# Kernel tuning notes

Hardware: AMD Instinct MI355X
Metric: run time of the kernel (lower is better)

The kernel has to match this reference:

```python
import jax, jax.numpy as jnp
import numpy as np

B, N, T, D = 256, 64, 60, 128
H = 128  # gate hidden dims


def setup_inputs() -> dict:
    key = jax.random.key(0)
    ks = jax.random.split(key, 5)
    x = jax.random.normal(ks[0], (B, N, T, D), dtype=jnp.float32)
    s = 1.0 / np.sqrt(D)
    sg_w1 = jax.random.normal(ks[1], (D, H), dtype=jnp.float32) * s
    sg_b1 = jnp.zeros((H,), dtype=jnp.float32)
    sg_w2 = jax.random.normal(ks[2], (H, 1), dtype=jnp.float32) * (1.0 / np.sqrt(H))
    sg_b2 = jnp.zeros((1,), dtype=jnp.float32)
    tg_w1 = jax.random.normal(ks[3], (D, H), dtype=jnp.float32) * s
    tg_b1 = jnp.zeros((H,), dtype=jnp.float32)
    tg_w2 = jax.random.normal(ks[4], (H, 1), dtype=jnp.float32) * (1.0 / np.sqrt(H))
    tg_b2 = jnp.zeros((1,), dtype=jnp.float32)
    return {"x": x, "sg_w1": sg_w1, "sg_b1": sg_b1, "sg_w2": sg_w2, "sg_b2": sg_b2,
            "tg_w1": tg_w1, "tg_b1": tg_b1, "tg_w2": tg_w2, "tg_b2": tg_b2}


def reference(x, sg_w1, sg_b1, sg_w2, sg_b2, tg_w1, tg_b1, tg_w2, tg_b2):
    # Spatial attentional aggregation, vectorized over all timesteps at once.
    # Segment softmax over batch_index == softmax over the node axis (regular segments).
    gate = jnp.tanh(x @ sg_w1 + sg_b1) @ sg_w2 + sg_b2          # [B, N, T, 1]
    alpha = jax.nn.softmax(gate, axis=1)                        # softmax over nodes
    pooled = jnp.sum(alpha * x, axis=1)                         # [B, T, D]
    # Temporal attention pooling over the sequence axis.
    score = jnp.tanh(pooled @ tg_w1 + tg_b1) @ tg_w2 + tg_b2    # [B, T, 1]
    tw = jax.nn.softmax(score, axis=1)                          # [B, T, 1]
    final = jnp.sum(tw * pooled, axis=1)                        # [B, D]
    return final, tw
```

## Files before the change

kernel.cpp:

```cpp
#include <hip/hip_runtime.h>

#define B_ 256
#define N_ 64
#define T_ 60
#define D_ 128
#define H_ 128

typedef __attribute__((ext_vector_type(8))) short short8;
typedef __attribute__((ext_vector_type(4))) float f32x4;

__device__ __forceinline__ unsigned short f2bf(float f) {
  unsigned int u = __builtin_bit_cast(unsigned int, f);
  u = u + 0x7FFFu + ((u >> 16) & 1u);
  return (unsigned short)(u >> 16);
}

__device__ __forceinline__ float tanh_fast(float x) {
  float e = __builtin_amdgcn_exp2f(x * 2.885390081777927f);
  return 1.0f - 2.0f * __builtin_amdgcn_rcpf(e + 1.0f);
}

__global__ __launch_bounds__(256) void prep_weights(
    const float* __restrict__ sg_w1, const float* __restrict__ tg_w1,
    unsigned short* __restrict__ wfrag) {
  int tid = blockIdx.x * 256 + threadIdx.x;
  if (tid >= 2 * 4 * 8 * 64) return;
  int l  = tid & 63;
  int nt = (tid >> 6) & 7;
  int kt = (tid >> 9) & 3;
  int m  = tid >> 11;
  const float* W = m ? tg_w1 : sg_w1;
  int n  = nt * 16 + (l & 15);
  int k0 = kt * 32 + 8 * (l >> 4);
  unsigned short* dst = wfrag + (size_t)tid * 8;
#pragma unroll
  for (int i = 0; i < 8; ++i) dst[i] = f2bf(W[(k0 + i) * H_ + n]);
}

__global__ __launch_bounds__(256, 4) void spatial_kernel(
    const float* __restrict__ x,
    const short8* __restrict__ wfrag,
    const float* __restrict__ b1,
    const float* __restrict__ w2,
    float* __restrict__ pooled) {
  __shared__ __align__(16) char xs16[64 * 272];
  __shared__ float gpart[2][64];

  const int tid = threadIdx.x;
  const int bid = blockIdx.x;
  const int b = bid / T_;
  const int t = bid - b * T_;

  const float* xb = x + (size_t)b * (N_ * T_ * D_) + (size_t)t * D_;

  const int cg  = tid >> 3;
  const int sub = tid & 7;

  float4 px[8];
#pragma unroll
  for (int r = 0; r < 8; ++r) {
    const int n = sub + 8 * r;
    px[r] = *(const float4*)(xb + (size_t)n * (T_ * D_) + 4 * cg);
  }
#pragma unroll
  for (int r = 0; r < 8; ++r) {
    const int n = sub + 8 * r;
    unsigned lo = ((unsigned)f2bf(px[r].y) << 16) | f2bf(px[r].x);
    unsigned hi = ((unsigned)f2bf(px[r].w) << 16) | f2bf(px[r].z);
    *(uint2*)(xs16 + n * 272 + cg * 8) = make_uint2(lo, hi);
  }
  __syncthreads();

  const int l  = tid & 63;
  const int w  = tid >> 6;
  const int lg = l >> 4;
  const int lr = l & 15;
  const int wr = w >> 1;
  const int wc = w & 1;

  float b1v[4], w2v[4];
#pragma unroll
  for (int ntl = 0; ntl < 4; ++ntl) {
    b1v[ntl] = b1[wc * 64 + ntl * 16 + lr];
    w2v[ntl] = w2[wc * 64 + ntl * 16 + lr];
  }

  f32x4 acc[2][4];
#pragma unroll
  for (int mt = 0; mt < 2; ++mt)
#pragma unroll
    for (int ntl = 0; ntl < 4; ++ntl) acc[mt][ntl] = (f32x4)(0.0f);

#pragma unroll
  for (int kt = 0; kt < 4; ++kt) {
#pragma unroll
    for (int mt = 0; mt < 2; ++mt) {
      const int row = 32 * wr + 16 * mt + lr;
      short8 af = *(const short8*)(xs16 + row * 272 + kt * 64 + lg * 16);
#pragma unroll
      for (int ntl = 0; ntl < 4; ++ntl) {
        short8 bf = wfrag[(kt * 8 + wc * 4 + ntl) * 64 + l];
        acc[mt][ntl] = __builtin_amdgcn_mfma_f32_16x16x32_bf16(af, bf, acc[mt][ntl], 0, 0, 0);
      }
    }
  }

#pragma unroll
  for (int mt = 0; mt < 2; ++mt) {
#pragma unroll
    for (int j = 0; j < 4; ++j) {
      float s = 0.f;
#pragma unroll
      for (int ntl = 0; ntl < 4; ++ntl) {
        float h = acc[mt][ntl][j] + b1v[ntl];
        s += tanh_fast(h) * w2v[ntl];
      }
      s += __shfl_xor(s, 1);
      s += __shfl_xor(s, 2);
      s += __shfl_xor(s, 4);
      s += __shfl_xor(s, 8);
      if (lr == 0) gpart[wc][32 * wr + 16 * mt + 4 * lg + j] = s;
    }
  }
  __syncthreads();

  float g = gpart[0][l] + gpart[1][l];
  float p = __builtin_amdgcn_exp2f(g * 1.4426950408889634f);
  float sm = p;
  sm += __shfl_xor(sm, 32);
  sm += __shfl_xor(sm, 16);
  sm += __shfl_xor(sm, 8);
  sm += __shfl_xor(sm, 4);
  sm += __shfl_xor(sm, 2);
  sm += __shfl_xor(sm, 1);
  const float alpha = p * __builtin_amdgcn_rcpf(sm);

  f32x4 q = (f32x4)(0.0f);
#pragma unroll
  for (int r = 0; r < 8; ++r) {
    const int n = sub + 8 * r;
    const float av = __shfl(alpha, n);
    q[0] += av * px[r].x;
    q[1] += av * px[r].y;
    q[2] += av * px[r].z;
    q[3] += av * px[r].w;
  }
#pragma unroll
  for (int m = 1; m <= 4; m <<= 1) {
    q[0] += __shfl_xor(q[0], m);
    q[1] += __shfl_xor(q[1], m);
    q[2] += __shfl_xor(q[2], m);
    q[3] += __shfl_xor(q[3], m);
  }
  if (sub == 0)
    *(f32x4*)(pooled + ((size_t)b * T_ + t) * D_ + 4 * cg) = q;
}

__global__ __launch_bounds__(256) void temporal_kernel(
    const float* __restrict__ pooled,
    const short8* __restrict__ wfrag,
    const float* __restrict__ b1,
    const float* __restrict__ w2,
    float* __restrict__ out) {
  __shared__ float xs[64][132];
  __shared__ float score_lds[64];
  __shared__ float tw_lds[64];
  __shared__ float pp[2][128];

  const int tid = threadIdx.x;
  const int b = blockIdx.x;

  const float* pb = pooled + (size_t)b * T_ * D_;
#pragma unroll
  for (int it = 0; it < 8; ++it) {
    int q = it * 256 + tid;
    int n = q >> 5;
    int c4 = (q & 31) << 2;
    float4 v = {0.f, 0.f, 0.f, 0.f};
    if (n < T_) v = *(const float4*)(pb + n * D_ + c4);
    *(float4*)(&xs[n][c4]) = v;
  }
  __syncthreads();

  const int l = tid & 63;
  const int w = tid >> 6;
  const int lg = l >> 4;
  const int lr = l & 15;

  float b1v[8], w2v[8];
#pragma unroll
  for (int nt = 0; nt < 8; ++nt) {
    b1v[nt] = b1[nt * 16 + lr];
    w2v[nt] = w2[nt * 16 + lr];
  }

  f32x4 acc[8];
#pragma unroll
  for (int nt = 0; nt < 8; ++nt) acc[nt] = (f32x4)(0.0f);

  const int row = 16 * w + lr;
#pragma unroll
  for (int kt = 0; kt < 4; ++kt) {
    const int k0 = kt * 32 + 8 * lg;
    float4 a0 = *(const float4*)(&xs[row][k0]);
    float4 a1 = *(const float4*)(&xs[row][k0 + 4]);
    short8 af;
    af[0] = (short)f2bf(a0.x); af[1] = (short)f2bf(a0.y);
    af[2] = (short)f2bf(a0.z); af[3] = (short)f2bf(a0.w);
    af[4] = (short)f2bf(a1.x); af[5] = (short)f2bf(a1.y);
    af[6] = (short)f2bf(a1.z); af[7] = (short)f2bf(a1.w);
#pragma unroll
    for (int nt = 0; nt < 8; ++nt) {
      short8 bf = wfrag[(kt * 8 + nt) * 64 + l];
      acc[nt] = __builtin_amdgcn_mfma_f32_16x16x32_bf16(af, bf, acc[nt], 0, 0, 0);
    }
  }

#pragma unroll
  for (int j = 0; j < 4; ++j) {
    float s = 0.f;
#pragma unroll
    for (int nt = 0; nt < 8; ++nt) {
      float h = acc[nt][j] + b1v[nt];
      s += tanh_fast(h) * w2v[nt];
    }
    s += __shfl_xor(s, 1);
    s += __shfl_xor(s, 2);
    s += __shfl_xor(s, 4);
    s += __shfl_xor(s, 8);
    if (lr == 0) score_lds[16 * w + 4 * lg + j] = s;
  }
  __syncthreads();

  float p = (l < T_) ? __builtin_amdgcn_exp2f(score_lds[l] * 1.4426950408889634f) : 0.f;
  float sm = p;
  sm += __shfl_xor(sm, 32);
  sm += __shfl_xor(sm, 16);
  sm += __shfl_xor(sm, 8);
  sm += __shfl_xor(sm, 4);
  sm += __shfl_xor(sm, 2);
  sm += __shfl_xor(sm, 1);
  float tw = p / sm;
  if (w == 0) {
    tw_lds[l] = tw;
    if (l < T_) out[B_ * D_ + b * T_ + l] = tw;
  }
  __syncthreads();

  const int c = tid & 127;
  const int hh = tid >> 7;
  float s = 0.f;
#pragma unroll
  for (int i = 0; i < 30; ++i) {
    int tt = 30 * hh + i;
    s += tw_lds[tt] * xs[tt][c];
  }
  pp[hh][c] = s;
  __syncthreads();
  if (tid < 128) out[(size_t)b * D_ + tid] = pp[0][tid] + pp[1][tid];
}

extern "C" void kernel_launch(void* const* d_in, const int* in_sizes, int n_in,
                              void* d_out, int out_size, void* d_ws, size_t ws_size,
                              hipStream_t stream) {
  const float* x     = (const float*)d_in[0];
  const float* sg_w1 = (const float*)d_in[1];
  const float* sg_b1 = (const float*)d_in[2];
  const float* sg_w2 = (const float*)d_in[3];
  const float* tg_w1 = (const float*)d_in[5];
  const float* tg_b1 = (const float*)d_in[6];
  const float* tg_w2 = (const float*)d_in[7];
  float* out = (float*)d_out;

  unsigned short* wfrag = (unsigned short*)d_ws;
  float* pooled = (float*)((char*)d_ws + 65536);

  prep_weights<<<16, 256, 0, stream>>>(sg_w1, tg_w1, wfrag);
  spatial_kernel<<<B_ * T_, 256, 0, stream>>>(
      x, (const short8*)wfrag, sg_b1, sg_w2, pooled);
  temporal_kernel<<<B_, 256, 0, stream>>>(
      pooled, (const short8*)(wfrag + 16384), tg_b1, tg_w2, out);
}
```

Measured before the change: 154.1 us.

## Process two timesteps per spatial block with contiguous 1KB row loads

Each spatial block now handles two adjacent timesteps with 512 threads, so every wave loads a full contiguous 1KB span (two t rows × 128 floats) per node instead of 512B fragments. Grid size is halved and the per-timestep work is split across wave groups. The shuffle-based alpha broadcast and cross-lane reduction are replaced by LDS arrays and a cross-wave reduction through shared memory. This adds LDS usage and extra barriers, which may reduce occupancy.

```diff
diff --git a/kernel.cpp b/kernel.cpp
--- a/kernel.cpp
+++ b/kernel.cpp
@@ -37,45 +37,46 @@
   for (int i = 0; i < 8; ++i) dst[i] = f2bf(W[(k0 + i) * H_ + n]);
 }
 
-__global__ __launch_bounds__(256, 4) void spatial_kernel(
+__global__ __launch_bounds__(512, 4) void spatial_kernel(
     const float* __restrict__ x,
     const short8* __restrict__ wfrag,
     const float* __restrict__ b1,
     const float* __restrict__ w2,
     float* __restrict__ pooled) {
-  __shared__ __align__(16) char xs16[64 * 272];
-  __shared__ float gpart[2][64];
+  __shared__ __align__(16) char xt16[2 * 17408];
+  __shared__ float gpart[2][2][64];
+  __shared__ float alph[2][64];
+  __shared__ f32x4 pp[8][64];
 
   const int tid = threadIdx.x;
   const int bid = blockIdx.x;
-  const int b = bid / T_;
-  const int t = bid - b * T_;
-
-  const float* xb = x + (size_t)b * (N_ * T_ * D_) + (size_t)t * D_;
-
-  const int cg  = tid >> 3;
-  const int sub = tid & 7;
-
+  const int b  = bid / (T_ / 2);
+  const int tc = bid - b * (T_ / 2);
+  const int t0 = 2 * tc;
+
+  const int w = tid >> 6;
+  const int l = tid & 63;
+
+  const float* xb = x + (size_t)b * (N_ * T_ * D_) + (size_t)t0 * D_;
   float4 px[8];
 #pragma unroll
-  for (int r = 0; r < 8; ++r) {
-    const int n = sub + 8 * r;
-    px[r] = *(const float4*)(xb + (size_t)n * (T_ * D_) + 4 * cg);
-  }
-#pragma unroll
-  for (int r = 0; r < 8; ++r) {
-    const int n = sub + 8 * r;
-    unsigned lo = ((unsigned)f2bf(px[r].y) << 16) | f2bf(px[r].x);
-    unsigned hi = ((unsigned)f2bf(px[r].w) << 16) | f2bf(px[r].z);
-    *(uint2*)(xs16 + n * 272 + cg * 8) = make_uint2(lo, hi);
-  }
-  __syncthreads();
-
-  const int l  = tid & 63;
-  const int w  = tid >> 6;
+  for (int j = 0; j < 8; ++j)
+    px[j] = *(const float4*)(xb + (size_t)(8 * j + w) * (T_ * D_) + 4 * l);
+
+  const int lt  = l >> 5;
+  const int d4  = l & 31;
+#pragma unroll
+  for (int j = 0; j < 8; ++j) {
+    unsigned lo = ((unsigned)f2bf(px[j].y) << 16) | f2bf(px[j].x);
+    unsigned hi = ((unsigned)f2bf(px[j].w) << 16) | f2bf(px[j].z);
+    *(uint2*)(xt16 + lt * 17408 + (8 * j + w) * 272 + d4 * 8) = make_uint2(lo, hi);
+  }
+  __syncthreads();
+
   const int lg = l >> 4;
   const int lr = l & 15;
-  const int wr = w >> 1;
+  const int tw = w >> 2;
+  const int wr = (w >> 1) & 1;
   const int wc = w & 1;
 
   float b1v[4], w2v[4];
@@ -96,7 +97,7 @@
 #pragma unroll
     for (int mt = 0; mt < 2; ++mt) {
       const int row = 32 * wr + 16 * mt + lr;
-      short8 af = *(const short8*)(xs16 + row * 272 + kt * 64 + lg * 16);
+      short8 af = *(const short8*)(xt16 + tw * 17408 + row * 272 + kt * 64 + lg * 16);
 #pragma unroll
       for (int ntl = 0; ntl < 4; ++ntl) {
         short8 bf = wfrag[(kt * 8 + wc * 4 + ntl) * 64 + l];
@@ -119,41 +120,43 @@
       s += __shfl_xor(s, 2);
       s += __shfl_xor(s, 4);
       s += __shfl_xor(s, 8);
-      if (lr == 0) gpart[wc][32 * wr + 16 * mt + 4 * lg + j] = s;
-    }
-  }
-  __syncthreads();
-
-  float g = gpart[0][l] + gpart[1][l];
-  float p = __builtin_amdgcn_exp2f(g * 1.4426950408889634f);
-  float sm = p;
-  sm += __shfl_xor(sm, 32);
-  sm += __shfl_xor(sm, 16);
-  sm += __shfl_xor(sm, 8);
-  sm += __shfl_xor(sm, 4);
-  sm += __shfl_xor(sm, 2);
-  sm += __shfl_xor(sm, 1);
-  const float alpha = p * __builtin_amdgcn_rcpf(sm);
+      if (lr == 0) gpart[tw][wc][32 * wr + 16 * mt + 4 * lg + j] = s;
+    }
+  }
+  __syncthreads();
+
+  if ((w & 3) == 0) {
+    float g = gpart[tw][0][l] + gpart[tw][1][l];
+    float p = __builtin_amdgcn_exp2f(g * 1.4426950408889634f);
+    float sm = p;
+    sm += __shfl_xor(sm, 32);
+    sm += __shfl_xor(sm, 16);
+    sm += __shfl_xor(sm, 8);
+    sm += __shfl_xor(sm, 4);
+    sm += __shfl_xor(sm, 2);
+    sm += __shfl_xor(sm, 1);
+    alph[tw][l] = p * __builtin_amdgcn_rcpf(sm);
+  }
+  __syncthreads();
 
   f32x4 q = (f32x4)(0.0f);
 #pragma unroll
-  for (int r = 0; r < 8; ++r) {
-    const int n = sub + 8 * r;
-    const float av = __shfl(alpha, n);
-    q[0] += av * px[r].x;
-    q[1] += av * px[r].y;
-    q[2] += av * px[r].z;
-    q[3] += av * px[r].w;
-  }
-#pragma unroll
-  for (int m = 1; m <= 4; m <<= 1) {
-    q[0] += __shfl_xor(q[0], m);
-    q[1] += __shfl_xor(q[1], m);
-    q[2] += __shfl_xor(q[2], m);
-    q[3] += __shfl_xor(q[3], m);
-  }
-  if (sub == 0)
-    *(f32x4*)(pooled + ((size_t)b * T_ + t) * D_ + 4 * cg) = q;
+  for (int j = 0; j < 8; ++j) {
+    const float av = alph[lt][8 * j + w];
+    q[0] += av * px[j].x;
+    q[1] += av * px[j].y;
+    q[2] += av * px[j].z;
+    q[3] += av * px[j].w;
+  }
+  pp[w][l] = q;
+  __syncthreads();
+
+  if (w == 0) {
+    f32x4 s4 = pp[0][l];
+#pragma unroll
+    for (int w2i = 1; w2i < 8; ++w2i) s4 += pp[w2i][l];
+    *(f32x4*)(pooled + ((size_t)b * T_ + t0 + lt) * D_ + 4 * d4) = s4;
+  }
 }
 
 __global__ __launch_bounds__(256) void temporal_kernel(
@@ -276,7 +279,7 @@
   float* pooled = (float*)((char*)d_ws + 65536);
 
   prep_weights<<<16, 256, 0, stream>>>(sg_w1, tg_w1, wfrag);
-  spatial_kernel<<<B_ * T_, 256, 0, stream>>>(
+  spatial_kernel<<<B_ * (T_ / 2), 512, 0, stream>>>(
       x, (const short8*)wfrag, sg_b1, sg_w2, pooled);
   temporal_kernel<<<B_, 256, 0, stream>>>(
       pooled, (const short8*)(wfrag + 16384), tg_b1, tg_w2, out);
```

New measurement: 150.3 us. 2.5% less time.

## Restructure spatial kernel into per-batch node-slab loop with streaming softmax

Applied to the files above, without the earlier changes.

Each spatial block now handles one batch and half of the nodes (32 slabs), iterating over node slabs where each slab covers all 60 timesteps. The next slab's x loads are double-buffered against the current MFMA and gating work. The softmax becomes an unnormalized exp-weighted accumulation with the denominator stored separately. The temporal kernel merges the two halves and normalizes. Gate weights are staged once in LDS per block instead of being re-read from global memory per timestep block. The grid shrinks from 15360 blocks to 512 with more sequential work each, which risks low occupancy/parallelism (2 blocks per CU). Dropping max-subtraction in the softmax risks overflow.

```diff
diff --git a/kernel.cpp b/kernel.cpp
--- a/kernel.cpp
+++ b/kernel.cpp
@@ -18,6 +18,12 @@
 __device__ __forceinline__ float tanh_fast(float x) {
   float e = __builtin_amdgcn_exp2f(x * 2.885390081777927f);
   return 1.0f - 2.0f * __builtin_amdgcn_rcpf(e + 1.0f);
+}
+
+__device__ __forceinline__ void lds_barrier() {
+  asm volatile("s_waitcnt lgkmcnt(0)" ::: "memory");
+  __builtin_amdgcn_s_barrier();
+  asm volatile("" ::: "memory");
 }
 
 __global__ __launch_bounds__(256) void prep_weights(
@@ -37,39 +43,33 @@
   for (int i = 0; i < 8; ++i) dst[i] = f2bf(W[(k0 + i) * H_ + n]);
 }
 
-__global__ __launch_bounds__(256, 4) void spatial_kernel(
+__global__ __launch_bounds__(256, 2) void spatial_kernel(
     const float* __restrict__ x,
-    const short8* __restrict__ wfrag,
+    const unsigned short* __restrict__ wfrag_g,
     const float* __restrict__ b1,
     const float* __restrict__ w2,
-    float* __restrict__ pooled) {
-  __shared__ __align__(16) char xs16[64 * 272];
+    float* __restrict__ acc_p,
+    float* __restrict__ den_p) {
+  __shared__ __align__(16) char tile[64 * 272];
+  __shared__ __align__(16) char wlds[32768];
   __shared__ float gpart[2][64];
 
   const int tid = threadIdx.x;
   const int bid = blockIdx.x;
-  const int b = bid / T_;
-  const int t = bid - b * T_;
-
-  const float* xb = x + (size_t)b * (N_ * T_ * D_) + (size_t)t * D_;
-
-  const int cg  = tid >> 3;
-  const int sub = tid & 7;
-
-  float4 px[8];
+  const int b  = bid >> 1;
+  const int nh = bid & 1;
+
+  const int sub = tid >> 5;
+  const int cg  = tid & 31;
+
+  const float* xb = x + (size_t)b * (N_ * T_ * D_) + (size_t)(nh * 32) * (T_ * D_);
+
+  int roff[8];
 #pragma unroll
   for (int r = 0; r < 8; ++r) {
-    const int n = sub + 8 * r;
-    px[r] = *(const float4*)(xb + (size_t)n * (T_ * D_) + 4 * cg);
-  }
-#pragma unroll
-  for (int r = 0; r < 8; ++r) {
-    const int n = sub + 8 * r;
-    unsigned lo = ((unsigned)f2bf(px[r].y) << 16) | f2bf(px[r].x);
-    unsigned hi = ((unsigned)f2bf(px[r].w) << 16) | f2bf(px[r].z);
-    *(uint2*)(xs16 + n * 272 + cg * 8) = make_uint2(lo, hi);
-  }
-  __syncthreads();
+    int t = 8 * r + sub;
+    roff[r] = (t > 59 ? 59 : t) * D_ + 4 * cg;
+  }
 
   const int l  = tid & 63;
   const int w  = tid >> 6;
@@ -85,79 +85,119 @@
     w2v[ntl] = w2[wc * 64 + ntl * 16 + lr];
   }
 
-  f32x4 acc[2][4];
-#pragma unroll
-  for (int mt = 0; mt < 2; ++mt)
-#pragma unroll
-    for (int ntl = 0; ntl < 4; ++ntl) acc[mt][ntl] = (f32x4)(0.0f);
-
-#pragma unroll
-  for (int kt = 0; kt < 4; ++kt) {
-#pragma unroll
-    for (int mt = 0; mt < 2; ++mt) {
-      const int row = 32 * wr + 16 * mt + lr;
-      short8 af = *(const short8*)(xs16 + row * 272 + kt * 64 + lg * 16);
-#pragma unroll
-      for (int ntl = 0; ntl < 4; ++ntl) {
-        short8 bf = wfrag[(kt * 8 + wc * 4 + ntl) * 64 + l];
-        acc[mt][ntl] = __builtin_amdgcn_mfma_f32_16x16x32_bf16(af, bf, acc[mt][ntl], 0, 0, 0);
-      }
-    }
-  }
-
-#pragma unroll
-  for (int mt = 0; mt < 2; ++mt) {
-#pragma unroll
-    for (int j = 0; j < 4; ++j) {
-      float s = 0.f;
-#pragma unroll
-      for (int ntl = 0; ntl < 4; ++ntl) {
-        float h = acc[mt][ntl][j] + b1v[ntl];
-        s += tanh_fast(h) * w2v[ntl];
-      }
-      s += __shfl_xor(s, 1);
-      s += __shfl_xor(s, 2);
-      s += __shfl_xor(s, 4);
-      s += __shfl_xor(s, 8);
-      if (lr == 0) gpart[wc][32 * wr + 16 * mt + 4 * lg + j] = s;
-    }
-  }
-  __syncthreads();
-
-  float g = gpart[0][l] + gpart[1][l];
-  float p = __builtin_amdgcn_exp2f(g * 1.4426950408889634f);
-  float sm = p;
-  sm += __shfl_xor(sm, 32);
-  sm += __shfl_xor(sm, 16);
-  sm += __shfl_xor(sm, 8);
-  sm += __shfl_xor(sm, 4);
-  sm += __shfl_xor(sm, 2);
-  sm += __shfl_xor(sm, 1);
-  const float alpha = p * __builtin_amdgcn_rcpf(sm);
-
-  f32x4 q = (f32x4)(0.0f);
+  float4 wtmp[8];
+#pragma unroll
+  for (int i = 0; i < 8; ++i)
+    wtmp[i] = *(const float4*)(wfrag_g + (size_t)(tid + 256 * i) * 8);
+
+  float4 pxA[8], pxB[8];
+#pragma unroll
+  for (int r = 0; r < 8; ++r) pxA[r] = *(const float4*)(xb + roff[r]);
+
+#pragma unroll
+  for (int i = 0; i < 8; ++i)
+    *(float4*)(wlds + (size_t)(tid + 256 * i) * 16) = wtmp[i];
+  lds_barrier();
+
+  f32x4 accr[8];
+  float denr[8];
+#pragma unroll
+  for (int r = 0; r < 8; ++r) { accr[r] = (f32x4)(0.0f); denr[r] = 0.0f; }
+
+#define SLAB_BODY(CUR, NXT, S)                                                  \
+  {                                                                             \
+                   \
+    if ((S) < 31) {                                                             \
+      const float* nsb = xb + (size_t)((S) + 1) * (T_ * D_);                    \
+      _Pragma("unroll")                                                         \
+      for (int r = 0; r < 8; ++r) NXT[r] = *(const float4*)(nsb + roff[r]);     \
+    }                                                                           \
+                                               \
+    _Pragma("unroll")                                                           \
+    for (int r = 0; r < 8; ++r) {                                               \
+      const int t = 8 * r + sub;                                                \
+      unsigned lo = ((unsigned)f2bf(CUR[r].y) << 16) | f2bf(CUR[r].x);          \
+      unsigned hi = ((unsigned)f2bf(CUR[r].w) << 16) | f2bf(CUR[r].z);          \
+      *(uint2*)(tile + t * 272 + cg * 8) = make_uint2(lo, hi);                  \
+    }                                                                           \
+    lds_barrier();                                                              \
+                           \
+    {                                                                           \
+      f32x4 macc[2][4];                                                         \
+      _Pragma("unroll")                                                         \
+      for (int mt = 0; mt < 2; ++mt)                                            \
+        _Pragma("unroll")                                                       \
+        for (int ntl = 0; ntl < 4; ++ntl) macc[mt][ntl] = (f32x4)(0.0f);        \
+      _Pragma("unroll")                                                         \
+      for (int kt = 0; kt < 4; ++kt) {                                          \
+        _Pragma("unroll")                                                       \
+        for (int mt = 0; mt < 2; ++mt) {                                        \
+          const int row = 32 * wr + 16 * mt + lr;                               \
+          short8 af = *(const short8*)(tile + row * 272 + kt * 64 + lg * 16);   \
+          _Pragma("unroll")                                                     \
+          for (int ntl = 0; ntl < 4; ++ntl) {                                   \
+            short8 bf = *(const short8*)(                                       \
+                wlds + ((kt * 8 + wc * 4 + ntl) * 64 + l) * 16);                \
+            macc[mt][ntl] = __builtin_amdgcn_mfma_f32_16x16x32_bf16(            \
+                af, bf, macc[mt][ntl], 0, 0, 0);                                \
+          }                                                                     \
+        }                                                                       \
+      }                                                                         \
+      _Pragma("unroll")                                                         \
+      for (int mt = 0; mt < 2; ++mt) {                                          \
+        _Pragma("unroll")                                                       \
+        for (int j = 0; j < 4; ++j) {                                           \
+          float sg = 0.f;                                                       \
+          _Pragma("unroll")                                                     \
+          for (int ntl = 0; ntl < 4; ++ntl) {                                   \
+            float h = macc[mt][ntl][j] + b1v[ntl];                              \
+            sg += tanh_fast(h) * w2v[ntl];                                      \
+          }                                                                     \
+          sg += __shfl_xor(sg, 1);                                              \
+          sg += __shfl_xor(sg, 2);                                              \
+          sg += __shfl_xor(sg, 4);                                              \
+          sg += __shfl_xor(sg, 8);                                              \
+          if (lr == 0) gpart[wc][32 * wr + 16 * mt + 4 * lg + j] = sg;          \
+        }                                                                       \
+      }                                                                         \
+    }                                                                           \
+    lds_barrier();                                                              \
+                    \
+    _Pragma("unroll")                                                           \
+    for (int r = 0; r < 8; ++r) {                                               \
+      const int t = 8 * r + sub;                                                \
+      float g = gpart[0][t] + gpart[1][t];                                      \
+      float e = __builtin_amdgcn_exp2f(g * 1.4426950408889634f);                \
+      accr[r][0] += e * CUR[r].x;                                               \
+      accr[r][1] += e * CUR[r].y;                                               \
+      accr[r][2] += e * CUR[r].z;                                               \
+      accr[r][3] += e * CUR[r].w;                                               \
+      denr[r] += e;                                                             \
+    }                                                                           \
+    lds_barrier();                                                              \
+  }
+
+  for (int sp = 0; sp < 16; ++sp) {
+    const int s0 = 2 * sp;
+    SLAB_BODY(pxA, pxB, s0);
+    SLAB_BODY(pxB, pxA, s0 + 1);
+  }
+#undef SLAB_BODY
+
 #pragma unroll
   for (int r = 0; r < 8; ++r) {
-    const int n = sub + 8 * r;
-    const float av = __shfl(alpha, n);
-    q[0] += av * px[r].x;
-    q[1] += av * px[r].y;
-    q[2] += av * px[r].z;
-    q[3] += av * px[r].w;
-  }
-#pragma unroll
-  for (int m = 1; m <= 4; m <<= 1) {
-    q[0] += __shfl_xor(q[0], m);
-    q[1] += __shfl_xor(q[1], m);
-    q[2] += __shfl_xor(q[2], m);
-    q[3] += __shfl_xor(q[3], m);
-  }
-  if (sub == 0)
-    *(f32x4*)(pooled + ((size_t)b * T_ + t) * D_ + 4 * cg) = q;
+    const int t = 8 * r + sub;
+    *(f32x4*)(acc_p + ((size_t)bid * 64 + t) * D_ + 4 * cg) = accr[r];
+  }
+  if (cg == 0) {
+#pragma unroll
+    for (int r = 0; r < 8; ++r) den_p[bid * 64 + 8 * r + sub] = denr[r];
+  }
 }
 
 __global__ __launch_bounds__(256) void temporal_kernel(
-    const float* __restrict__ pooled,
+    const float* __restrict__ acc_p,
+    const float* __restrict__ den_p,
     const short8* __restrict__ wfrag,
     const float* __restrict__ b1,
     const float* __restrict__ w2,
@@ -170,14 +210,25 @@
   const int tid = threadIdx.x;
   const int b = blockIdx.x;
 
-  const float* pb = pooled + (size_t)b * T_ * D_;
+  const float* a0 = acc_p + (size_t)(2 * b) * (64 * D_);
+  const float* a1 = a0 + 64 * D_;
+  const float* d0 = den_p + (2 * b) * 64;
+  const float* d1 = d0 + 64;
 #pragma unroll
   for (int it = 0; it < 8; ++it) {
     int q = it * 256 + tid;
     int n = q >> 5;
     int c4 = (q & 31) << 2;
     float4 v = {0.f, 0.f, 0.f, 0.f};
-    if (n < T_) v = *(const float4*)(pb + n * D_ + c4);
+    if (n < T_) {
+      float4 v0 = *(const float4*)(a0 + n * D_ + c4);
+      float4 v1 = *(const float4*)(a1 + n * D_ + c4);
+      float inv = __builtin_amdgcn_rcpf(d0[n] + d1[n]);
+      v.x = (v0.x + v1.x) * inv;
+      v.y = (v0.y + v1.y) * inv;
+      v.z = (v0.z + v1.z) * inv;
+      v.w = (v0.w + v1.w) * inv;
+    }
     *(float4*)(&xs[n][c4]) = v;
   }
   __syncthreads();
@@ -202,13 +253,13 @@
 #pragma unroll
   for (int kt = 0; kt < 4; ++kt) {
     const int k0 = kt * 32 + 8 * lg;
-    float4 a0 = *(const float4*)(&xs[row][k0]);
-    float4 a1 = *(const float4*)(&xs[row][k0 + 4]);
+    float4 a0v = *(const float4*)(&xs[row][k0]);
+    float4 a1v = *(const float4*)(&xs[row][k0 + 4]);
     short8 af;
-    af[0] = (short)f2bf(a0.x); af[1] = (short)f2bf(a0.y);
-    af[2] = (short)f2bf(a0.z); af[3] = (short)f2bf(a0.w);
-    af[4] = (short)f2bf(a1.x); af[5] = (short)f2bf(a1.y);
-    af[6] = (short)f2bf(a1.z); af[7] = (short)f2bf(a1.w);
+    af[0] = (short)f2bf(a0v.x); af[1] = (short)f2bf(a0v.y);
+    af[2] = (short)f2bf(a0v.z); af[3] = (short)f2bf(a0v.w);
+    af[4] = (short)f2bf(a1v.x); af[5] = (short)f2bf(a1v.y);
+    af[6] = (short)f2bf(a1v.z); af[7] = (short)f2bf(a1v.w);
 #pragma unroll
     for (int nt = 0; nt < 8; ++nt) {
       short8 bf = wfrag[(kt * 8 + nt) * 64 + l];
@@ -273,11 +324,12 @@
   float* out = (float*)d_out;
 
   unsigned short* wfrag = (unsigned short*)d_ws;
-  float* pooled = (float*)((char*)d_ws + 65536);
+  float* acc_p = (float*)((char*)d_ws + 65536);
+  float* den_p = (float*)((char*)d_ws + 65536 + 16777216);
 
   prep_weights<<<16, 256, 0, stream>>>(sg_w1, tg_w1, wfrag);
-  spatial_kernel<<<B_ * T_, 256, 0, stream>>>(
-      x, (const short8*)wfrag, sg_b1, sg_w2, pooled);
+  spatial_kernel<<<B_ * 2, 256, 0, stream>>>(
+      x, wfrag, sg_b1, sg_w2, acc_p, den_p);
   temporal_kernel<<<B_, 256, 0, stream>>>(
-      pooled, (const short8*)(wfrag + 16384), tg_b1, tg_w2, out);
-}
+      acc_p, den_p, (const short8*)(wfrag + 16384), tg_b1, tg_w2, out);
+}
```

New measurement: 145.0 us, median of 2. 1.06x faster.
